# Kernel optimization log

Measured on AMD Instinct MI355X. Metric: run time of the kernel, lower is better.

The kernel has to match this reference:

```python
import jax, jax.numpy as jnp
import numpy as np

N_EXPERTS, TOP_K, D_MODEL, D_INNER = 8, 2, 512, 2048
N, P = 4, 2048


def setup_inputs() -> dict:
    key = jax.random.key(0)
    k1, k2, k3 = jax.random.split(key, 3)
    # xavier_uniform on (E, d_model, d_inner): fan_in=d_model*d_inner, fan_out=E*d_inner
    bound_w = float(np.sqrt(6.0 / (D_MODEL * D_INNER + N_EXPERTS * D_INNER)))
    expert_weights = jax.random.uniform(k1, (N_EXPERTS, D_MODEL, D_INNER), jnp.float32, -bound_w, bound_w)
    expert_biases = jnp.zeros((N_EXPERTS, D_INNER), jnp.float32)
    # nn.Linear(d_model, n_experts) default init: U(-1/sqrt(fan_in), 1/sqrt(fan_in))
    bound_g = float(1.0 / np.sqrt(D_MODEL))
    gating_w = jax.random.uniform(k2, (N_EXPERTS, D_MODEL), jnp.float32, -bound_g, bound_g)
    gating_b = jax.random.uniform(k3, (N_EXPERTS,), jnp.float32, -bound_g, bound_g)
    sequences = jax.random.normal(jax.random.key(1), (N, P, D_MODEL), jnp.float32)
    return {
        "sequences": sequences,
        "expert_weights": expert_weights,
        "expert_biases": expert_biases,
        "gating_w": gating_w,
        "gating_b": gating_b,
    }


def reference(sequences, expert_weights, expert_biases, gating_w, gating_b):
    n, p, d = sequences.shape
    x = sequences.reshape(-1, d)                      # [T, d_model]
    T = x.shape[0]
    gates = jax.nn.softmax(x @ gating_w.T + gating_b, axis=-1)  # [T, E]
    top_v, top_i = jax.lax.top_k(gates, TOP_K)        # [T, K]
    # Scatter top-k gate values into a dense [T, E] gate matrix (zeros elsewhere).
    gfull = jnp.zeros_like(gates).at[jnp.arange(T)[:, None], top_i].set(top_v)
    # out_t = (1/K) * sum_e gfull[t,e] * (x_t @ W_e + b_e)  -- same math as the
    # per-token gathered bmm in the original, without materializing [T, d, h].
    out = jnp.einsum('te,td,edh->th', gfull, x, expert_weights)
    out = out + gfull @ expert_biases
    out = out / TOP_K
    return out.reshape(n, p, D_INNER)
```

## Files before the change

kernel.cpp:

```cpp
#include <hip/hip_runtime.h>
#include <hip/hip_bf16.h>

#define TT 8192
#define DM 512
#define DH 2048
#define NE 8
#define GB_TOK 16

typedef short short8 __attribute__((ext_vector_type(8)));
typedef short short4b __attribute__((ext_vector_type(4)));
typedef float f32x4  __attribute__((ext_vector_type(4)));

#define GL16(g, l) __builtin_amdgcn_global_load_lds(                          \
    (const __attribute__((address_space(1))) void*)(g),                       \
    (__attribute__((address_space(3))) void*)(l), 16, 0, 0)

__device__ __forceinline__ short f2bf(float f) {
    __hip_bfloat16 h = __float2bfloat16(f);
    return *reinterpret_cast<short*>(&h);
}

__global__ __launch_bounds__(256) void moe_gating(
    const float* __restrict__ x, const float* __restrict__ gw,
    const float* __restrict__ gb, int* __restrict__ counts,
    int* __restrict__ slot_list, float* __restrict__ w_list,
    short* __restrict__ xb)
{
    __shared__ float xs[4][DM];
    __shared__ int   ent_e[2 * GB_TOK];
    __shared__ int   ent_t[2 * GB_TOK];
    __shared__ float ent_w[2 * GB_TOK];
    __shared__ int   rank_s[2 * GB_TOK];
    __shared__ int   base_s[NE];

    const int wv = threadIdx.x >> 6, ln = threadIdx.x & 63;
    const int e = ln & 7, g = ln >> 3;
    const float* wp = gw + e * DM;

#pragma unroll
    for (int it = 0; it < GB_TOK / 4; ++it) {
        const int t = blockIdx.x * GB_TOK + wv * (GB_TOK / 4) + it;
        const float* xp = x + (size_t)t * DM;
        short* xbrow = xb + (size_t)t * DM;
        for (int i = ln; i < DM; i += 64) {
            const float v = xp[i];
            xs[wv][i] = v;
            xbrow[i] = f2bf(v);
        }
        __syncthreads();

        float acc = 0.f;
#pragma unroll 8
        for (int j = 0; j < 64; ++j) {
            const int d = g + (j << 3);
            acc = fmaf(xs[wv][d], wp[d], acc);
        }
        acc += __shfl_xor(acc, 8);
        acc += __shfl_xor(acc, 16);
        acc += __shfl_xor(acc, 32);
        const float logit = acc + gb[e];

        float lg[8];
#pragma unroll
        for (int j = 0; j < 8; ++j) lg[j] = __shfl(logit, j);

        if (ln == 0) {
            float m = lg[0];
#pragma unroll
            for (int j = 1; j < 8; ++j) m = fmaxf(m, lg[j]);
            float s = 0.f, ex[8];
#pragma unroll
            for (int j = 0; j < 8; ++j) { ex[j] = expf(lg[j] - m); s += ex[j]; }
            int i0 = 0;
#pragma unroll
            for (int j = 1; j < 8; ++j) if (lg[j] > lg[i0]) i0 = j;
            int i1 = (i0 == 0) ? 1 : 0;
#pragma unroll
            for (int j = 0; j < 8; ++j) if (j != i0 && lg[j] > lg[i1]) i1 = j;
            const float inv = 0.5f / s;
            const int sl = (wv * (GB_TOK / 4) + it) << 1;
            ent_e[sl]     = i0; ent_t[sl]     = (t << 1);     ent_w[sl]     = ex[i0] * inv;
            ent_e[sl + 1] = i1; ent_t[sl + 1] = (t << 1) | 1; ent_w[sl + 1] = ex[i1] * inv;
        }
        __syncthreads();
    }

    if (threadIdx.x < NE) {
        const int me = threadIdx.x;
        int n = 0;
        for (int i = 0; i < 2 * GB_TOK; ++i)
            if (ent_e[i] == me) rank_s[i] = n++;
        base_s[me] = n ? atomicAdd(&counts[me << 4], n) : 0;
    }
    __syncthreads();
    if (threadIdx.x < 2 * GB_TOK) {
        const int i = threadIdx.x;
        const int ee = ent_e[i];
        const int pos = ee * TT + base_s[ee] + rank_s[i];
        slot_list[pos] = ent_t[i];
        w_list[pos]    = ent_w[i];
    }
}

__global__ __launch_bounds__(256) void moe_wt(
    const float* __restrict__ W, short* __restrict__ Wt)
{
    __shared__ float t[64][65];
    const int e = blockIdx.z, n0 = blockIdx.x << 6, k0 = blockIdx.y << 6;
    const float* src = W + ((size_t)e * DM + k0) * DH + n0;
#pragma unroll
    for (int i = 0; i < 16; ++i) {
        const int idx = i * 256 + threadIdx.x;
        const int kk = idx >> 6, nn = idx & 63;
        t[kk][nn] = src[(size_t)kk * DH + nn];
    }
    __syncthreads();
    short* dst = Wt + ((size_t)e * DH + n0) * DM + k0;
#pragma unroll
    for (int i = 0; i < 4; ++i) {
        const int nn = i * 16 + (threadIdx.x >> 4);
        const int kk = (threadIdx.x & 15) << 2;
        short4b v;
#pragma unroll
        for (int c = 0; c < 4; ++c) v[c] = f2bf(t[kk + c][nn]);
        *(short4b*)&dst[(size_t)nn * DM + kk] = v;
    }
}

template <int GPATH>
__global__ __launch_bounds__(256) void moe_gemm_mfma(
    const short* __restrict__ xb, const short* __restrict__ Wt,
    const float* __restrict__ Bb, const int* __restrict__ counts,
    const int* __restrict__ slot_list, const float* __restrict__ w_list,
    float* __restrict__ G, float* __restrict__ out)
{
    const int e = blockIdx.z;
    const int cnt = counts[e << 4];
    const int row0 = blockIdx.y << 7;
    if (row0 >= cnt) return;
    const int rem = cnt - row0;
    const int h0 = blockIdx.x << 7;

    __shared__ short As[128 * 64];
    __shared__ short Bs[128 * 64];
    __shared__ int   slot_s[128];
    __shared__ float wgt_s[128];

    const int tid = threadIdx.x;
    if (tid < 128) {
        const int ok = tid < rem;
        slot_s[tid] = ok ? slot_list[e * TT + row0 + tid] : 0;
        wgt_s[tid]  = ok ? w_list[e * TT + row0 + tid] : 0.f;
    }
    __syncthreads();

    const int wid = tid >> 6, lane = tid & 63;
    const int wm = wid >> 1, wn = wid & 1;

    int a_srcoff[4], b_srcoff[4];
#pragma unroll
    for (int i = 0; i < 4; ++i) {
        const int c = i * 256 + wid * 64 + lane;
        const int r = c >> 3, cc = c & 7;
        const int tok = slot_s[r] >> 1;
        a_srcoff[i] = tok * DM + (((cc ^ (r & 7)) << 3));
        b_srcoff[i] = (h0 + r) * DM + (((cc ^ (r & 7)) << 3));
    }
    const short* We = Wt + (size_t)e * DH * DM;

    f32x4 acc[4][4];
#pragma unroll
    for (int mi = 0; mi < 4; ++mi)
#pragma unroll
        for (int ni = 0; ni < 4; ++ni)
            acc[mi][ni] = (f32x4){0.f, 0.f, 0.f, 0.f};

    for (int k0 = 0; k0 < DM; k0 += 64) {
        __syncthreads();
#pragma unroll
        for (int i = 0; i < 4; ++i) {
            const int dbase = (i * 256 + wid * 64) << 3;
            GL16(xb + a_srcoff[i] + k0, As + dbase);
            GL16(We + b_srcoff[i] + k0, Bs + dbase);
        }
        __syncthreads();

#pragma unroll
        for (int kk = 0; kk < 2; ++kk) {
            short8 a[4], b[4];
#pragma unroll
            for (int mi = 0; mi < 4; ++mi) {
                const int r = wm * 64 + mi * 16 + (lane & 15);
                const int c = kk * 4 + (lane >> 4);
                a[mi] = *(const short8*)&As[r * 64 + ((c ^ (r & 7)) << 3)];
            }
#pragma unroll
            for (int ni = 0; ni < 4; ++ni) {
                const int r = wn * 64 + ni * 16 + (lane & 15);
                const int c = kk * 4 + (lane >> 4);
                b[ni] = *(const short8*)&Bs[r * 64 + ((c ^ (r & 7)) << 3)];
            }
#pragma unroll
            for (int mi = 0; mi < 4; ++mi)
#pragma unroll
                for (int ni = 0; ni < 4; ++ni)
                    acc[mi][ni] = __builtin_amdgcn_mfma_f32_16x16x32_bf16(
                        a[mi], b[ni], acc[mi][ni], 0, 0, 0);
        }
    }

    const float* be = Bb + e * DH;
#pragma unroll
    for (int mi = 0; mi < 4; ++mi) {
#pragma unroll
        for (int r = 0; r < 4; ++r) {
            const int rl = wm * 64 + mi * 16 + (lane >> 4) * 4 + r;
            if (rl < rem) {
                const float w = wgt_s[rl];
                const int slot = slot_s[rl];
#pragma unroll
                for (int ni = 0; ni < 4; ++ni) {
                    const int col = h0 + wn * 64 + ni * 16 + (lane & 15);
                    const float v = w * (acc[mi][ni][r] + be[col]);
                    if (GPATH)
                        G[(size_t)slot * DH + col] = v;
                    else
                        unsafeAtomicAdd(&out[(size_t)(slot >> 1) * DH + col], v);
                }
            }
        }
    }
}

__global__ __launch_bounds__(256) void moe_combine(
    const float* __restrict__ G, float* __restrict__ out)
{
    const int n4 = TT * DH / 4;
    for (int i = blockIdx.x * 256 + threadIdx.x; i < n4; i += gridDim.x * 256) {
        const int f = i << 2;
        const int t = f >> 11;
        const int h = f & 2047;
        const float4 a = *(const float4*)&G[((size_t)(t << 1)) * DH + h];
        const float4 b = *(const float4*)&G[((size_t)(t << 1) + 1) * DH + h];
        float4 o;
        o.x = a.x + b.x; o.y = a.y + b.y; o.z = a.z + b.z; o.w = a.w + b.w;
        *(float4*)&out[f] = o;
    }
}

extern "C" void kernel_launch(void* const* d_in, const int* in_sizes, int n_in,
                              void* d_out, int out_size, void* d_ws, size_t ws_size,
                              hipStream_t stream) {
    const float* seq = (const float*)d_in[0];
    const float* ew  = (const float*)d_in[1];
    const float* eb  = (const float*)d_in[2];
    const float* gw  = (const float*)d_in[3];
    const float* gb  = (const float*)d_in[4];
    float* out = (float*)d_out;

    char* ws = (char*)d_ws;
    size_t off = 0;
    int* counts = (int*)(ws + off);           off += 1024;
    int* slot_list = (int*)(ws + off);        off += (size_t)NE * TT * 4;
    float* w_list = (float*)(ws + off);       off += (size_t)NE * TT * 4;
    short* xb = (short*)(ws + off);           off += (size_t)TT * DM * 2;
    short* Wt = (short*)(ws + off);           off += (size_t)NE * DH * DM * 2;
    float* G = (float*)(ws + off);
    const size_t need_g = off + (size_t)TT * 2 * DH * 4;
    const int gpath = (ws_size >= need_g);

    hipMemsetAsync(counts, 0, 1024, stream);
    if (!gpath)
        hipMemsetAsync(out, 0, (size_t)TT * DH * sizeof(float), stream);

    moe_gating<<<TT / GB_TOK, 256, 0, stream>>>(seq, gw, gb, counts, slot_list,
                                                w_list, xb);
    moe_wt<<<dim3(DH / 64, DM / 64, NE), 256, 0, stream>>>(ew, Wt);

    dim3 grid(DH / 128, TT / 128, NE);
    if (gpath) {
        moe_gemm_mfma<1><<<grid, 256, 0, stream>>>(xb, Wt, eb, counts, slot_list,
                                                   w_list, G, out);
        moe_combine<<<2048, 256, 0, stream>>>(G, out);
    } else {
        moe_gemm_mfma<0><<<grid, 256, 0, stream>>>(xb, Wt, eb, counts, slot_list,
                                                   w_list, G, out);
    }
}
```

Measured before the change: 262.4 us.

## Double-buffer GEMM LDS tiles and store per-slot expert outputs in bf16

The MFMA expert GEMM now double-buffers its A and B shared-memory tiles. It issues the global-to-LDS loads for the next k-tile before computing the current one and uses a single barrier per iteration. The intermediate per-slot buffer G is stored as bf16 instead of fp32, and the combine kernel reads bf16 pairs and widens them before summing. This halves the write and read traffic on G. The cost is doubled LDS per block, which can reduce occupancy, and extra rounding of the gated expert outputs before they are summed.

```diff
diff --git a/kernel.cpp b/kernel.cpp
--- a/kernel.cpp
+++ b/kernel.cpp
@@ -18,6 +18,11 @@
 __device__ __forceinline__ short f2bf(float f) {
     __hip_bfloat16 h = __float2bfloat16(f);
     return *reinterpret_cast<short*>(&h);
+}
+__device__ __forceinline__ float bf2f(short s) {
+    union { unsigned u; float f; } v;
+    v.u = ((unsigned)(unsigned short)s) << 16;
+    return v.f;
 }
 
 __global__ __launch_bounds__(256) void moe_gating(
@@ -132,7 +137,7 @@
     const short* __restrict__ xb, const short* __restrict__ Wt,
     const float* __restrict__ Bb, const int* __restrict__ counts,
     const int* __restrict__ slot_list, const float* __restrict__ w_list,
-    float* __restrict__ G, float* __restrict__ out)
+    short* __restrict__ G, float* __restrict__ out)
 {
     const int e = blockIdx.z;
     const int cnt = counts[e << 4];
@@ -141,8 +146,8 @@
     const int rem = cnt - row0;
     const int h0 = blockIdx.x << 7;
 
-    __shared__ short As[128 * 64];
-    __shared__ short Bs[128 * 64];
+    __shared__ short As[2][128 * 64];
+    __shared__ short Bs[2][128 * 64];
     __shared__ int   slot_s[128];
     __shared__ float wgt_s[128];
 
@@ -157,7 +162,7 @@
     const int wid = tid >> 6, lane = tid & 63;
     const int wm = wid >> 1, wn = wid & 1;
 
-    int a_srcoff[4], b_srcoff[4];
+    int a_srcoff[4], b_srcoff[4], dbase[4];
 #pragma unroll
     for (int i = 0; i < 4; ++i) {
         const int c = i * 256 + wid * 64 + lane;
@@ -165,6 +170,7 @@
         const int tok = slot_s[r] >> 1;
         a_srcoff[i] = tok * DM + (((cc ^ (r & 7)) << 3));
         b_srcoff[i] = (h0 + r) * DM + (((cc ^ (r & 7)) << 3));
+        dbase[i] = (i * 256 + wid * 64) << 3;
     }
     const short* We = Wt + (size_t)e * DH * DM;
 
@@ -175,39 +181,51 @@
         for (int ni = 0; ni < 4; ++ni)
             acc[mi][ni] = (f32x4){0.f, 0.f, 0.f, 0.f};
 
-    for (int k0 = 0; k0 < DM; k0 += 64) {
+#define STAGE(buf, k0)                                                        \
+    _Pragma("unroll")                                                         \
+    for (int i = 0; i < 4; ++i) {                                             \
+        GL16(xb + a_srcoff[i] + (k0), &As[buf][dbase[i]]);                    \
+        GL16(We + b_srcoff[i] + (k0), &Bs[buf][dbase[i]]);                    \
+    }
+
+#define COMPUTE(buf)                                                          \
+    _Pragma("unroll")                                                         \
+    for (int kk = 0; kk < 2; ++kk) {                                          \
+        short8 a[4], b[4];                                                    \
+        _Pragma("unroll")                                                     \
+        for (int mi = 0; mi < 4; ++mi) {                                      \
+            const int r = wm * 64 + mi * 16 + (lane & 15);                    \
+            const int c = kk * 4 + (lane >> 4);                               \
+            a[mi] = *(const short8*)&As[buf][r * 64 + ((c ^ (r & 7)) << 3)];  \
+        }                                                                     \
+        _Pragma("unroll")                                                     \
+        for (int ni = 0; ni < 4; ++ni) {                                      \
+            const int r = wn * 64 + ni * 16 + (lane & 15);                    \
+            const int c = kk * 4 + (lane >> 4);                               \
+            b[ni] = *(const short8*)&Bs[buf][r * 64 + ((c ^ (r & 7)) << 3)];  \
+        }                                                                     \
+        _Pragma("unroll")                                                     \
+        for (int mi = 0; mi < 4; ++mi)                                        \
+            _Pragma("unroll")                                                 \
+            for (int ni = 0; ni < 4; ++ni)                                    \
+                acc[mi][ni] = __builtin_amdgcn_mfma_f32_16x16x32_bf16(        \
+                    a[mi], b[ni], acc[mi][ni], 0, 0, 0);                      \
+    }
+
+    STAGE(0, 0)
+    __syncthreads();
+
+#pragma unroll
+    for (int kt = 0; kt < (DM / 64) - 1; ++kt) {
+        const int cur = kt & 1;
+        STAGE(cur ^ 1, (kt + 1) * 64)
+        COMPUTE(cur)
         __syncthreads();
-#pragma unroll
-        for (int i = 0; i < 4; ++i) {
-            const int dbase = (i * 256 + wid * 64) << 3;
-            GL16(xb + a_srcoff[i] + k0, As + dbase);
-            GL16(We + b_srcoff[i] + k0, Bs + dbase);
-        }
-        __syncthreads();
-
-#pragma unroll
-        for (int kk = 0; kk < 2; ++kk) {
-            short8 a[4], b[4];
-#pragma unroll
-            for (int mi = 0; mi < 4; ++mi) {
-                const int r = wm * 64 + mi * 16 + (lane & 15);
-                const int c = kk * 4 + (lane >> 4);
-                a[mi] = *(const short8*)&As[r * 64 + ((c ^ (r & 7)) << 3)];
-            }
-#pragma unroll
-            for (int ni = 0; ni < 4; ++ni) {
-                const int r = wn * 64 + ni * 16 + (lane & 15);
-                const int c = kk * 4 + (lane >> 4);
-                b[ni] = *(const short8*)&Bs[r * 64 + ((c ^ (r & 7)) << 3)];
-            }
-#pragma unroll
-            for (int mi = 0; mi < 4; ++mi)
-#pragma unroll
-                for (int ni = 0; ni < 4; ++ni)
-                    acc[mi][ni] = __builtin_amdgcn_mfma_f32_16x16x32_bf16(
-                        a[mi], b[ni], acc[mi][ni], 0, 0, 0);
-        }
-    }
+    }
+    COMPUTE(((DM / 64) - 1) & 1)
+
+#undef STAGE
+#undef COMPUTE
 
     const float* be = Bb + e * DH;
 #pragma unroll
@@ -223,7 +241,7 @@
                     const int col = h0 + wn * 64 + ni * 16 + (lane & 15);
                     const float v = w * (acc[mi][ni][r] + be[col]);
                     if (GPATH)
-                        G[(size_t)slot * DH + col] = v;
+                        G[(size_t)slot * DH + col] = f2bf(v);
                     else
                         unsafeAtomicAdd(&out[(size_t)(slot >> 1) * DH + col], v);
                 }
@@ -233,18 +251,26 @@
 }
 
 __global__ __launch_bounds__(256) void moe_combine(
-    const float* __restrict__ G, float* __restrict__ out)
+    const short* __restrict__ G, float* __restrict__ out)
 {
-    const int n4 = TT * DH / 4;
-    for (int i = blockIdx.x * 256 + threadIdx.x; i < n4; i += gridDim.x * 256) {
-        const int f = i << 2;
+    const int n8 = TT * DH / 8;
+    for (int i = blockIdx.x * 256 + threadIdx.x; i < n8; i += gridDim.x * 256) {
+        const int f = i << 3;
         const int t = f >> 11;
         const int h = f & 2047;
-        const float4 a = *(const float4*)&G[((size_t)(t << 1)) * DH + h];
-        const float4 b = *(const float4*)&G[((size_t)(t << 1) + 1) * DH + h];
-        float4 o;
-        o.x = a.x + b.x; o.y = a.y + b.y; o.z = a.z + b.z; o.w = a.w + b.w;
-        *(float4*)&out[f] = o;
+        const short8 a = *(const short8*)&G[((size_t)(t << 1)) * DH + h];
+        const short8 b = *(const short8*)&G[((size_t)(t << 1) + 1) * DH + h];
+        float4 o0, o1;
+        o0.x = bf2f(a[0]) + bf2f(b[0]);
+        o0.y = bf2f(a[1]) + bf2f(b[1]);
+        o0.z = bf2f(a[2]) + bf2f(b[2]);
+        o0.w = bf2f(a[3]) + bf2f(b[3]);
+        o1.x = bf2f(a[4]) + bf2f(b[4]);
+        o1.y = bf2f(a[5]) + bf2f(b[5]);
+        o1.z = bf2f(a[6]) + bf2f(b[6]);
+        o1.w = bf2f(a[7]) + bf2f(b[7]);
+        *(float4*)&out[f]     = o0;
+        *(float4*)&out[f + 4] = o1;
     }
 }
 
@@ -265,8 +291,8 @@
     float* w_list = (float*)(ws + off);       off += (size_t)NE * TT * 4;
     short* xb = (short*)(ws + off);           off += (size_t)TT * DM * 2;
     short* Wt = (short*)(ws + off);           off += (size_t)NE * DH * DM * 2;
-    float* G = (float*)(ws + off);
-    const size_t need_g = off + (size_t)TT * 2 * DH * 4;
+    short* G = (short*)(ws + off);
+    const size_t need_g = off + (size_t)TT * 2 * DH * 2;
     const int gpath = (ws_size >= need_g);
 
     hipMemsetAsync(counts, 0, 1024, stream);
@@ -281,7 +307,7 @@
     if (gpath) {
         moe_gemm_mfma<1><<<grid, 256, 0, stream>>>(xb, Wt, eb, counts, slot_list,
                                                    w_list, G, out);
-        moe_combine<<<2048, 256, 0, stream>>>(G, out);
+        moe_combine<<<1024, 256, 0, stream>>>(G, out);
     } else {
         moe_gemm_mfma<0><<<grid, 256, 0, stream>>>(xb, Wt, eb, counts, slot_list,
                                                    w_list, G, out);
```

New measurement: 235.3 us. -10.3%, faster.
